# Kernel optimization log

Measured on AMD Instinct MI355X. Metric: run time of the kernel, lower is better.

The kernel has to match this reference:

```python
import jax, jax.numpy as jnp
import numpy as np

EPS = 1e-12  # torch F.normalize clamp
D = 4        # max_displacement


def _l2norm_c(x):
    # L2 normalize over channel dim (axis=1), matching F.normalize(p=2, dim=1)
    n = jnp.sqrt(jnp.sum(x * x, axis=1, keepdims=True))
    return x / jnp.maximum(n, EPS)


def setup_inputs() -> dict:
    key = jax.random.key(0)
    k1, k2 = jax.random.split(key)
    B, C, H, W = 4, 128, 128, 256
    feat1 = jax.random.normal(k1, (B, C, H, W), dtype=jnp.float32)
    feat2_warped = jax.random.normal(k2, (B, C, H, W), dtype=jnp.float32)
    return {"feat1": feat1, "feat2_warped": feat2_warped}


def reference(feat1, feat2_warped):
    B, C, H, W = feat1.shape
    f1 = _l2norm_c(feat1)
    f2 = _l2norm_c(feat2_warped)
    # zero-pad spatial dims by D (matches F.unfold padding=D)
    f2p = jnp.pad(f2, ((0, 0), (0, 0), (D, D), (D, D)))
    costs = []
    # fixed (2D+1)^2 = 81 displacements, row-major (dy, dx) to match unfold ordering
    for dy in range(2 * D + 1):
        for dx in range(2 * D + 1):
            shifted = jax.lax.slice(f2p, (0, 0, dy, dx), (B, C, dy + H, dx + W))
            costs.append(jnp.sum(f1 * shifted, axis=1) / C)  # (B,H,W)
    cost = jnp.stack(costs, axis=1)  # (B, 81, H, W)
    return jax.nn.leaky_relu(cost, negative_slope=0.1)
```

## Files before the change

kernel.cpp:

```cpp
#include <hip/hip_runtime.h>

#define B_ 4
#define C_ 128
#define H_ 128
#define W_ 256
#define HW_ (H_ * W_)
#define ND 81
#define TH 8
#define TW 16
#define HR 16
#define WCOL 32
#define KC 32
#define NCHUNK (C_ / KC)
#define NTHREADS 512
#define BUFSZ 40960
#define F1OFF 32768

typedef short bf16x8 __attribute__((ext_vector_type(8)));
typedef float f32x4 __attribute__((ext_vector_type(4)));
typedef unsigned int u32x4 __attribute__((ext_vector_type(4)));

__device__ __forceinline__ int slotswz(int px, int slot) {
    return px * 64 + ((slot ^ (px & 3) ^ ((px >> 2) & 3)) * 16);
}

__device__ __forceinline__ unsigned int cvt_pk_bf16(float a, float b) {
    unsigned int r;
    asm("v_cvt_pk_bf16_f32 %0, %1, %2" : "=v"(r) : "v"(a), "v"(b));
    return r;
}

__device__ __forceinline__ void dot2_sq(unsigned int u, float& ss) {
    asm("v_dot2_f32_bf16 %0, %1, %1, %0" : "+v"(ss) : "v"(u));
}

#define BARRIER()                                             \
    do {                                                      \
        asm volatile("s_waitcnt lgkmcnt(0)" ::: "memory");    \
        __builtin_amdgcn_s_barrier();                         \
    } while (0)

__global__ __launch_bounds__(NTHREADS)
void corr81_kernel(const float* __restrict__ f1g, const float* __restrict__ f2g,
                   float* __restrict__ out) {
    __shared__ __align__(16) char lds[2][BUFSZ];
    char* ldsc = &lds[0][0];
    float* invn2 = (float*)&lds[0][0];
    float* invn1 = (float*)&lds[0][2048];

    const int tid  = threadIdx.x;
    const int lane = tid & 63;
    const int wave = tid >> 6;
    const int col  = lane & 15;
    const int quad = lane >> 4;

    const int flat = blockIdx.x + 16 * blockIdx.y + 256 * blockIdx.z;
    const int orig = (flat & 7) * 128 + (flat >> 3);
    const int w0 = (orig & 15) * TW;
    const int h0 = ((orig >> 4) & 15) * TH;
    const int b  = orig >> 8;
    const float* f2base = f2g + (size_t)b * C_ * HW_;
    const float* f1base = f1g + (size_t)b * C_ * HW_;

    const int hh2 = tid >> 5, ww2 = tid & 31;
    const int gh2 = h0 - 4 + hh2, gw2 = w0 - 4 + ww2;
    const bool v2 = (gh2 >= 0) && (gh2 < H_) && (gw2 >= 0) && (gw2 < W_);
    const int offs2 = v2 ? (gh2 * W_ + gw2) : 0;
    int wa[4];
#pragma unroll
    for (int s = 0; s < 4; ++s) wa[s] = slotswz(tid, s);

    const int px1w = tid >> 2, q1 = tid & 3;
    const int offs1 = (h0 + (px1w >> 4)) * W_ + (w0 + (px1w & 15)) + q1 * 8 * HW_;
    const int w1a = F1OFF + slotswz(px1w, q1);

    const int slotr = (quad ^ (col & 3) ^ ((col >> 2) & 3)) * 16;
    const int rb2 = wave * 2048 + col * 64 + slotr;
    const int rb1 = F1OFF + (wave * 16 + col) * 64 + slotr;

    f32x4 acc[9][2];
#pragma unroll
    for (int d = 0; d < 9; ++d) { acc[d][0] = (f32x4)0.f; acc[d][1] = (f32x4)0.f; }

    f32x4 A[8] = {};
    f32x4 F[2] = {};
    float ss2a = 0.f, ss2b = 0.f, ss1 = 0.f;

#define ISSUE_F2(kc0)                                                           \
    if (v2) {                                                                   \
        _Pragma("unroll")                                                       \
        for (int c = 0; c < 32; ++c)                                            \
            A[c >> 2][c & 3] = (f2base + (size_t)((kc0) + c) * HW_)[offs2];     \
    }

#define ISSUE_F1(kc0)                                                           \
    {                                                                           \
        _Pragma("unroll")                                                       \
        for (int j = 0; j < 8; ++j)                                             \
            F[j >> 2][j & 3] = (f1base + (size_t)((kc0) + j) * HW_)[offs1];     \
    }

#define PACK_F2(buf)                                                            \
    {                                                                           \
        _Pragma("unroll")                                                       \
        for (int s = 0; s < 4; ++s) {                                           \
            u32x4 U;                                                            \
            U[0] = cvt_pk_bf16(A[s * 2][0], A[s * 2][1]);                       \
            U[1] = cvt_pk_bf16(A[s * 2][2], A[s * 2][3]);                       \
            U[2] = cvt_pk_bf16(A[s * 2 + 1][0], A[s * 2 + 1][1]);               \
            U[3] = cvt_pk_bf16(A[s * 2 + 1][2], A[s * 2 + 1][3]);               \
            dot2_sq(U[0], ss2a); dot2_sq(U[1], ss2b);                           \
            dot2_sq(U[2], ss2a); dot2_sq(U[3], ss2b);                           \
            *(u32x4*)(ldsc + (buf) * BUFSZ + wa[s]) = U;                        \
        }                                                                       \
    }

#define PACK_F1(buf)                                                            \
    {                                                                           \
        u32x4 U;                                                                \
        U[0] = cvt_pk_bf16(F[0][0], F[0][1]);                                   \
        U[1] = cvt_pk_bf16(F[0][2], F[0][3]);                                   \
        U[2] = cvt_pk_bf16(F[1][0], F[1][1]);                                   \
        U[3] = cvt_pk_bf16(F[1][2], F[1][3]);                                   \
        dot2_sq(U[0], ss1); dot2_sq(U[1], ss1);                                 \
        dot2_sq(U[2], ss1); dot2_sq(U[3], ss1);                                 \
        *(u32x4*)(ldsc + (buf) * BUFSZ + w1a) = U;                              \
    }

#define MFMA_PHASE(buf)                                                         \
    {                                                                           \
        const char* rb = ldsc + (buf) * BUFSZ;                                  \
        bf16x8 af = *(const bf16x8*)(rb + rb1);                                 \
        _Pragma("unroll")                                                       \
        for (int dy = 0; dy < 9; ++dy) {                                        \
            bf16x8 b0 = *(const bf16x8*)(rb + rb2 + dy * 2048);                 \
            bf16x8 b1 = *(const bf16x8*)(rb + rb2 + dy * 2048 + 1024);          \
            acc[dy][0] = __builtin_amdgcn_mfma_f32_16x16x32_bf16(af, b0, acc[dy][0], 0, 0, 0); \
            acc[dy][1] = __builtin_amdgcn_mfma_f32_16x16x32_bf16(af, b1, acc[dy][1], 0, 0, 0); \
        }                                                                       \
    }

    ISSUE_F2(0); ISSUE_F1(0);
    PACK_F2(0);  PACK_F1(0);
    ISSUE_F2(KC); ISSUE_F1(KC);
    BARRIER();

#pragma unroll
    for (int k = 0; k < NCHUNK; ++k) {
        const int bk = k & 1;
        MFMA_PHASE(bk);
        if (k < NCHUNK - 1) {
            PACK_F2(bk ^ 1); PACK_F1(bk ^ 1);
            if (k < NCHUNK - 2) { ISSUE_F2((k + 2) * KC); ISSUE_F1((k + 2) * KC); }
            BARRIER();
        }
    }

    invn2[tid] = 1.f / fmaxf(sqrtf(ss2a + ss2b), 1e-12f);
    float t1 = ss1 + __shfl_xor(ss1, 1);
    t1 += __shfl_xor(t1, 2);
    if (q1 == 0) invn1[px1w] = 1.f / fmaxf(sqrtf(t1), 1e-12f);
    BARRIER();

    const int hOut = h0 + wave;
    float* outB = out + (size_t)b * ND * HW_ + (size_t)hOut * W_;
    const float scale = 1.f / (float)C_;

#pragma unroll
    for (int dy = 0; dy < 9; ++dy) {
        int hr = wave + dy;
#pragma unroll
        for (int t = 0; t < 2; ++t) {
            float i2 = invn2[hr * WCOL + t * 16 + col];
#pragma unroll
            for (int r = 0; r < 4; ++r) {
                int row = quad * 4 + r;
                int dx = t * 16 + col - row;
                if (dx >= 0 && dx <= 8) {
                    float v = acc[dy][t][r] * invn1[wave * 16 + row] * i2 * scale;
                    v = (v >= 0.f) ? v : 0.1f * v;
                    outB[(size_t)(dy * 9 + dx) * HW_ + (w0 + row)] = v;
                }
            }
        }
    }
#undef ISSUE_F2
#undef ISSUE_F1
#undef PACK_F2
#undef PACK_F1
#undef MFMA_PHASE
}

extern "C" void kernel_launch(void* const* d_in, const int* in_sizes, int n_in,
                              void* d_out, int out_size, void* d_ws, size_t ws_size,
                              hipStream_t stream) {
    const float* f1 = (const float*)d_in[0];
    const float* f2 = (const float*)d_in[1];
    float* out = (float*)d_out;
    dim3 grid(W_ / TW, H_ / TH, B_);
    corr81_kernel<<<grid, NTHREADS, 0, stream>>>(f1, f2, out);
}
```

Baseline: 67.92 us.

## Split block into producer and MFMA consumer waves with half-height tiles

Restructures the kernel so four waves only load, convert and normalize-sum tiles into LDS while four other waves only run the MFMA correlation and the epilogue. Output tile height drops from 8 to 4 rows, which doubles the grid and shrinks LDS per block. The aim is to overlap global loads with matrix math across waves and raise occupancy. The cost is a larger halo-to-interior ratio, with more redundant f2 reads per output, and only half the waves doing MFMA work.

```diff
diff --git a/kernel.cpp b/kernel.cpp
--- a/kernel.cpp
+++ b/kernel.cpp
@@ -6,15 +6,14 @@
 #define W_ 256
 #define HW_ (H_ * W_)
 #define ND 81
-#define TH 8
+#define TH 4
 #define TW 16
-#define HR 16
-#define WCOL 32
+#define HR2 12
 #define KC 32
 #define NCHUNK (C_ / KC)
 #define NTHREADS 512
-#define BUFSZ 40960
-#define F1OFF 32768
+#define F1OFF (HR2 * 32 * 64)
+#define BUFSZ (F1OFF + 64 * 64)
 
 typedef short bf16x8 __attribute__((ext_vector_type(8)));
 typedef float f32x4 __attribute__((ext_vector_type(4)));
@@ -44,151 +43,162 @@
 void corr81_kernel(const float* __restrict__ f1g, const float* __restrict__ f2g,
                    float* __restrict__ out) {
     __shared__ __align__(16) char lds[2][BUFSZ];
-    char* ldsc = &lds[0][0];
     float* invn2 = (float*)&lds[0][0];
-    float* invn1 = (float*)&lds[0][2048];
+    float* invn1 = (float*)&lds[0][1536];
 
     const int tid  = threadIdx.x;
-    const int lane = tid & 63;
     const int wave = tid >> 6;
-    const int col  = lane & 15;
-    const int quad = lane >> 4;
-
-    const int flat = blockIdx.x + 16 * blockIdx.y + 256 * blockIdx.z;
-    const int orig = (flat & 7) * 128 + (flat >> 3);
+
+    const int flat = blockIdx.x + 16 * blockIdx.y + 512 * blockIdx.z;
+    const int orig = (flat & 7) * 256 + (flat >> 3);
     const int w0 = (orig & 15) * TW;
-    const int h0 = ((orig >> 4) & 15) * TH;
-    const int b  = orig >> 8;
-    const float* f2base = f2g + (size_t)b * C_ * HW_;
-    const float* f1base = f1g + (size_t)b * C_ * HW_;
-
-    const int hh2 = tid >> 5, ww2 = tid & 31;
-    const int gh2 = h0 - 4 + hh2, gw2 = w0 - 4 + ww2;
-    const bool v2 = (gh2 >= 0) && (gh2 < H_) && (gw2 >= 0) && (gw2 < W_);
-    const int offs2 = v2 ? (gh2 * W_ + gw2) : 0;
-    int wa[4];
-#pragma unroll
-    for (int s = 0; s < 4; ++s) wa[s] = slotswz(tid, s);
-
-    const int px1w = tid >> 2, q1 = tid & 3;
-    const int offs1 = (h0 + (px1w >> 4)) * W_ + (w0 + (px1w & 15)) + q1 * 8 * HW_;
-    const int w1a = F1OFF + slotswz(px1w, q1);
-
-    const int slotr = (quad ^ (col & 3) ^ ((col >> 2) & 3)) * 16;
-    const int rb2 = wave * 2048 + col * 64 + slotr;
-    const int rb1 = F1OFF + (wave * 16 + col) * 64 + slotr;
-
-    f32x4 acc[9][2];
-#pragma unroll
-    for (int d = 0; d < 9; ++d) { acc[d][0] = (f32x4)0.f; acc[d][1] = (f32x4)0.f; }
-
-    f32x4 A[8] = {};
-    f32x4 F[2] = {};
-    float ss2a = 0.f, ss2b = 0.f, ss1 = 0.f;
-
-#define ISSUE_F2(kc0)                                                           \
-    if (v2) {                                                                   \
-        _Pragma("unroll")                                                       \
-        for (int c = 0; c < 32; ++c)                                            \
-            A[c >> 2][c & 3] = (f2base + (size_t)((kc0) + c) * HW_)[offs2];     \
-    }
-
-#define ISSUE_F1(kc0)                                                           \
-    {                                                                           \
-        _Pragma("unroll")                                                       \
-        for (int j = 0; j < 8; ++j)                                             \
-            F[j >> 2][j & 3] = (f1base + (size_t)((kc0) + j) * HW_)[offs1];     \
-    }
-
-#define PACK_F2(buf)                                                            \
-    {                                                                           \
-        _Pragma("unroll")                                                       \
-        for (int s = 0; s < 4; ++s) {                                           \
-            u32x4 U;                                                            \
-            U[0] = cvt_pk_bf16(A[s * 2][0], A[s * 2][1]);                       \
-            U[1] = cvt_pk_bf16(A[s * 2][2], A[s * 2][3]);                       \
-            U[2] = cvt_pk_bf16(A[s * 2 + 1][0], A[s * 2 + 1][1]);               \
-            U[3] = cvt_pk_bf16(A[s * 2 + 1][2], A[s * 2 + 1][3]);               \
-            dot2_sq(U[0], ss2a); dot2_sq(U[1], ss2b);                           \
-            dot2_sq(U[2], ss2a); dot2_sq(U[3], ss2b);                           \
-            *(u32x4*)(ldsc + (buf) * BUFSZ + wa[s]) = U;                        \
-        }                                                                       \
-    }
-
-#define PACK_F1(buf)                                                            \
-    {                                                                           \
-        u32x4 U;                                                                \
-        U[0] = cvt_pk_bf16(F[0][0], F[0][1]);                                   \
-        U[1] = cvt_pk_bf16(F[0][2], F[0][3]);                                   \
-        U[2] = cvt_pk_bf16(F[1][0], F[1][1]);                                   \
-        U[3] = cvt_pk_bf16(F[1][2], F[1][3]);                                   \
-        dot2_sq(U[0], ss1); dot2_sq(U[1], ss1);                                 \
-        dot2_sq(U[2], ss1); dot2_sq(U[3], ss1);                                 \
-        *(u32x4*)(ldsc + (buf) * BUFSZ + w1a) = U;                              \
-    }
-
-#define MFMA_PHASE(buf)                                                         \
-    {                                                                           \
-        const char* rb = ldsc + (buf) * BUFSZ;                                  \
-        bf16x8 af = *(const bf16x8*)(rb + rb1);                                 \
-        _Pragma("unroll")                                                       \
-        for (int dy = 0; dy < 9; ++dy) {                                        \
-            bf16x8 b0 = *(const bf16x8*)(rb + rb2 + dy * 2048);                 \
-            bf16x8 b1 = *(const bf16x8*)(rb + rb2 + dy * 2048 + 1024);          \
-            acc[dy][0] = __builtin_amdgcn_mfma_f32_16x16x32_bf16(af, b0, acc[dy][0], 0, 0, 0); \
-            acc[dy][1] = __builtin_amdgcn_mfma_f32_16x16x32_bf16(af, b1, acc[dy][1], 0, 0, 0); \
-        }                                                                       \
-    }
-
-    ISSUE_F2(0); ISSUE_F1(0);
-    PACK_F2(0);  PACK_F1(0);
-    ISSUE_F2(KC); ISSUE_F1(KC);
-    BARRIER();
-
-#pragma unroll
-    for (int k = 0; k < NCHUNK; ++k) {
-        const int bk = k & 1;
-        MFMA_PHASE(bk);
-        if (k < NCHUNK - 1) {
-            PACK_F2(bk ^ 1); PACK_F1(bk ^ 1);
-            if (k < NCHUNK - 2) { ISSUE_F2((k + 2) * KC); ISSUE_F1((k + 2) * KC); }
+    const int h0 = ((orig >> 4) & 31) * TH;
+    const int b  = orig >> 9;
+    const float* f2b = f2g + (size_t)b * C_ * HW_;
+    const float* f1b = f1g + (size_t)b * C_ * HW_;
+
+    if (wave < 4) {
+        const int lane = tid & 63;
+        const int col  = lane & 15;
+        const int quad = lane >> 4;
+        const int w = wave;
+        const int slotr = (quad ^ (col & 3) ^ ((col >> 2) & 3)) * 16;
+        const int rb2 = w * 2048 + col * 64 + slotr;
+        const int rb1 = F1OFF + (w * 16 + col) * 64 + slotr;
+
+        f32x4 acc[9][2];
+#pragma unroll
+        for (int d = 0; d < 9; ++d) { acc[d][0] = (f32x4)0.f; acc[d][1] = (f32x4)0.f; }
+
+        BARRIER();
+
+#pragma unroll
+        for (int k = 0; k < NCHUNK; ++k) {
+            const char* base = &lds[k & 1][0];
+            bf16x8 af = *(const bf16x8*)(base + rb1);
+#pragma unroll
+            for (int dy = 0; dy < 9; ++dy) {
+                bf16x8 b0 = *(const bf16x8*)(base + rb2 + dy * 2048);
+                bf16x8 b1 = *(const bf16x8*)(base + rb2 + dy * 2048 + 1024);
+                acc[dy][0] = __builtin_amdgcn_mfma_f32_16x16x32_bf16(af, b0, acc[dy][0], 0, 0, 0);
+                acc[dy][1] = __builtin_amdgcn_mfma_f32_16x16x32_bf16(af, b1, acc[dy][1], 0, 0, 0);
+            }
             BARRIER();
         }
-    }
-
-    invn2[tid] = 1.f / fmaxf(sqrtf(ss2a + ss2b), 1e-12f);
-    float t1 = ss1 + __shfl_xor(ss1, 1);
-    t1 += __shfl_xor(t1, 2);
-    if (q1 == 0) invn1[px1w] = 1.f / fmaxf(sqrtf(t1), 1e-12f);
-    BARRIER();
-
-    const int hOut = h0 + wave;
-    float* outB = out + (size_t)b * ND * HW_ + (size_t)hOut * W_;
-    const float scale = 1.f / (float)C_;
-
-#pragma unroll
-    for (int dy = 0; dy < 9; ++dy) {
-        int hr = wave + dy;
-#pragma unroll
-        for (int t = 0; t < 2; ++t) {
-            float i2 = invn2[hr * WCOL + t * 16 + col];
-#pragma unroll
-            for (int r = 0; r < 4; ++r) {
-                int row = quad * 4 + r;
-                int dx = t * 16 + col - row;
-                if (dx >= 0 && dx <= 8) {
-                    float v = acc[dy][t][r] * invn1[wave * 16 + row] * i2 * scale;
-                    v = (v >= 0.f) ? v : 0.1f * v;
-                    outB[(size_t)(dy * 9 + dx) * HW_ + (w0 + row)] = v;
+
+        const int hOut = h0 + w;
+        float* outB = out + (size_t)b * ND * HW_ + (size_t)hOut * W_;
+        const float scale = 1.f / (float)C_;
+#pragma unroll
+        for (int dy = 0; dy < 9; ++dy) {
+            int hr = w + dy;
+#pragma unroll
+            for (int t = 0; t < 2; ++t) {
+                float i2 = invn2[hr * 32 + t * 16 + col];
+#pragma unroll
+                for (int r = 0; r < 4; ++r) {
+                    int row = quad * 4 + r;
+                    int dx = t * 16 + col - row;
+                    if (dx >= 0 && dx <= 8) {
+                        float v = acc[dy][t][r] * invn1[w * 16 + row] * i2 * scale;
+                        v = (v >= 0.f) ? v : 0.1f * v;
+                        outB[(size_t)(dy * 9 + dx) * HW_ + (w0 + row)] = v;
+                    }
                 }
             }
         }
+    } else {
+        const int st = tid - 256;
+        const bool isf2 = st < 192;
+        const int ww  = st & 31;
+        const int hhA = st >> 5;
+        const int gw  = w0 - 4 + ww;
+        const bool okW = (gw >= 0) && (gw < W_);
+        const int ghA = h0 - 4 + hhA, ghB = ghA + 6;
+        const bool vA = isf2 && okW && (ghA >= 0) && (ghA < H_);
+        const bool vB = isf2 && okW && (ghB >= 0) && (ghB < H_);
+        const int offA = vA ? (ghA * W_ + gw) : 0;
+        const int offB = vB ? (ghB * W_ + gw) : 0;
+        const int pxA = st, pxB = 192 + st;
+        const int px1 = st - 192;
+        const int off1 = (h0 + (px1 >> 4)) * W_ + (w0 + (px1 & 15));
+
+        int waA[4], waB[4];
+#pragma unroll
+        for (int s = 0; s < 4; ++s) {
+            waA[s] = isf2 ? slotswz(pxA, s) : (F1OFF + slotswz(px1, s));
+            waB[s] = slotswz(pxB & 511, s);
+        }
+
+        f32x4 RA[8] = {}, RB[8] = {};
+        float ssA = 0.f, ssB = 0.f;
+
+#define S_ISSUE(kc0)                                                          \
+        if (isf2) {                                                           \
+            _Pragma("unroll")                                                 \
+            for (int c = 0; c < 32; ++c) {                                    \
+                RA[c >> 2][c & 3] = vA ? f2b[(size_t)((kc0) + c) * HW_ + offA] : 0.f; \
+                RB[c >> 2][c & 3] = vB ? f2b[(size_t)((kc0) + c) * HW_ + offB] : 0.f; \
+            }                                                                 \
+        } else {                                                              \
+            _Pragma("unroll")                                                 \
+            for (int c = 0; c < 32; ++c)                                      \
+                RA[c >> 2][c & 3] = f1b[(size_t)((kc0) + c) * HW_ + off1];    \
+        }
+
+#define S_PACK(buf)                                                           \
+        {                                                                     \
+            char* base = &lds[(buf)][0];                                      \
+            _Pragma("unroll")                                                 \
+            for (int s = 0; s < 4; ++s) {                                     \
+                u32x4 U;                                                      \
+                U[0] = cvt_pk_bf16(RA[s * 2][0], RA[s * 2][1]);               \
+                U[1] = cvt_pk_bf16(RA[s * 2][2], RA[s * 2][3]);               \
+                U[2] = cvt_pk_bf16(RA[s * 2 + 1][0], RA[s * 2 + 1][1]);       \
+                U[3] = cvt_pk_bf16(RA[s * 2 + 1][2], RA[s * 2 + 1][3]);       \
+                dot2_sq(U[0], ssA); dot2_sq(U[1], ssA);                       \
+                dot2_sq(U[2], ssA); dot2_sq(U[3], ssA);                       \
+                *(u32x4*)(base + waA[s]) = U;                                 \
+            }                                                                 \
+            if (isf2) {                                                       \
+                _Pragma("unroll")                                             \
+                for (int s = 0; s < 4; ++s) {                                 \
+                    u32x4 U;                                                  \
+                    U[0] = cvt_pk_bf16(RB[s * 2][0], RB[s * 2][1]);           \
+                    U[1] = cvt_pk_bf16(RB[s * 2][2], RB[s * 2][3]);           \
+                    U[2] = cvt_pk_bf16(RB[s * 2 + 1][0], RB[s * 2 + 1][1]);   \
+                    U[3] = cvt_pk_bf16(RB[s * 2 + 1][2], RB[s * 2 + 1][3]);   \
+                    dot2_sq(U[0], ssB); dot2_sq(U[1], ssB);                   \
+                    dot2_sq(U[2], ssB); dot2_sq(U[3], ssB);                   \
+                    *(u32x4*)(base + waB[s]) = U;                             \
+                }                                                             \
+            }                                                                 \
+        }
+
+        S_ISSUE(0);
+        S_PACK(0);
+        S_ISSUE(KC);
+        BARRIER();
+
+#pragma unroll
+        for (int k = 0; k < NCHUNK; ++k) {
+            if (k < NCHUNK - 1) {
+                S_PACK((k + 1) & 1);
+                if (k < NCHUNK - 2) S_ISSUE((k + 2) * KC);
+            } else {
+                float iA = 1.f / fmaxf(sqrtf(ssA), 1e-12f);
+                if (isf2) {
+                    invn2[pxA] = iA;
+                    invn2[pxB] = 1.f / fmaxf(sqrtf(ssB), 1e-12f);
+                } else {
+                    invn1[px1] = iA;
+                }
+            }
+            BARRIER();
+        }
+#undef S_ISSUE
+#undef S_PACK
     }
-#undef ISSUE_F2
-#undef ISSUE_F1
-#undef PACK_F2
-#undef PACK_F1
-#undef MFMA_PHASE
 }
 
 extern "C" void kernel_launch(void* const* d_in, const int* in_sizes, int n_in,
```

New measurement: 90.64 us. +33.4%, slower.
